# Kernel optimization log

Hardware: AMD Instinct MI355X
Metric: run time of the kernel (lower is better)

Reference implementation:

```python
import jax, jax.numpy as jnp
import numpy as np

B, T, C, H = 32, 512, 8, 256  # batch, seq_len, n_channels, HIDDEN_SIZE
G = 4 * H  # gate dim (i, f, g, o)


def setup_inputs() -> dict:
    key = jax.random.key(0)
    ks = jax.random.split(key, 12)
    k_scale = 1.0 / np.sqrt(H)  # PyTorch LSTM/Linear uniform init bound
    u = lambda k, shape: jax.random.uniform(k, shape, jnp.float32, -k_scale, k_scale)
    return {
        "x": jax.random.normal(ks[0], (B, T, C), jnp.float32),
        # per-channel LSTM layer 1 (input_size=1)
        "Wih1": u(ks[1], (C, G, 1)),
        "Whh1": u(ks[2], (C, G, H)),
        "bih1": u(ks[3], (C, G)),
        "bhh1": u(ks[4], (C, G)),
        # per-channel LSTM layer 2 (input_size=H)
        "Wih2": u(ks[5], (C, G, H)),
        "Whh2": u(ks[6], (C, G, H)),
        "bih2": u(ks[7], (C, G)),
        "bhh2": u(ks[8], (C, G)),
        # per-channel Linear(H, 1)
        "Wlin": u(ks[9], (C, H)),
        "blin": u(ks[10], (C,)),
    }


def _lstm_layer(x_proj, Whh):
    """x_proj: [T, C, B, 4H] precomputed input projection + biases.
    Whh: [C, 4H, H]. Returns hidden states [T, C, B, H]."""
    c_dim, b_dim = x_proj.shape[1], x_proj.shape[2]
    h0 = jnp.zeros((c_dim, b_dim, H), x_proj.dtype)
    c0 = jnp.zeros((c_dim, b_dim, H), x_proj.dtype)

    def step(carry, xp_t):
        h, c = carry
        gates = xp_t + jnp.einsum('cbh,cgh->cbg', h, Whh)
        i, f, g, o = jnp.split(gates, 4, axis=-1)  # PyTorch gate order i,f,g,o
        i = jax.nn.sigmoid(i)
        f = jax.nn.sigmoid(f)
        g = jnp.tanh(g)
        o = jax.nn.sigmoid(o)
        c_new = f * c + i * g
        h_new = o * jnp.tanh(c_new)
        return (h_new, c_new), h_new

    _, hs = jax.lax.scan(step, (h0, c0), x_proj)
    return hs  # [T, C, B, H]


def reference(x, Wih1, Whh1, bih1, bhh1, Wih2, Whh2, bih2, bhh2, Wlin, blin):
    # Dropout layers are identity in eval mode.
    # Layer 1: input_size=1 -> input projection is a per-channel scale of x.
    b1 = (bih1 + bhh1)[None, :, None, :]  # [1, C, 1, 4H]
    xp1 = jnp.einsum('btc,cg->tcbg', x, Wih1[:, :, 0]) + b1  # [T, C, B, 4H]
    h1 = _lstm_layer(xp1, Whh1)  # [T, C, B, H]

    # Layer 2
    b2 = (bih2 + bhh2)[None, :, None, :]
    xp2 = jnp.einsum('tcbh,cgh->tcbg', h1, Wih2) + b2
    h2 = _lstm_layer(xp2, Whh2)  # [T, C, B, H]

    # Per-channel Linear(H, 1), concatenated over channel dim.
    out = jnp.einsum('tcbh,ch->btc', h2, Wlin) + blin[None, None, :]
    return out  # [B, T, C]
```

## Files before the change

### kernel.cpp

```cpp
#include <hip/hip_runtime.h>

#define Bn 32
#define Tn 512
#define Cn 8
#define Hn 256
#define Gn 1024
#define NTHR 256
#define SLC  16
#define NBLK (Cn*2*SLC)
#define K2n  (Hn/2)
#define BUFS 4
#define EXU  (BUFS*Cn*K2n*Bn)
#define GP2  18

typedef __attribute__((ext_vector_type(8))) __bf16 bf16x8;
typedef __attribute__((ext_vector_type(8))) short  short8;
typedef __attribute__((ext_vector_type(4))) float  f32x4;
typedef __attribute__((ext_vector_type(4))) unsigned uintx4;
typedef unsigned long long u64;

__device__ __forceinline__ unsigned bfr(float f) {
    unsigned u = __float_as_uint(f);
    return (u + 0x7fffu + ((u >> 16) & 1u)) >> 16;
}
__device__ __forceinline__ float sigmf(float v)  { return 1.0f / (1.0f + __expf(-v)); }
__device__ __forceinline__ float tanh_f(float v) { return 1.0f - 2.0f / (__expf(2.0f * v) + 1.0f); }

__device__ __forceinline__ f32x4 mf(short8 a, short8 b, f32x4 c) {
    return __builtin_amdgcn_mfma_f32_16x16x32_bf16(
        __builtin_bit_cast(bf16x8, a), __builtin_bit_cast(bf16x8, b), c, 0, 0, 0);
}

__device__ __forceinline__ void splitw(const float* __restrict__ p, short8& hi, short8& lo) {
    short8 h, l;
#pragma unroll
    for (int j = 0; j < 8; ++j) {
        const float v = p[j];
        const unsigned hb = bfr(v);
        h[j] = (short)hb;
        l[j] = (short)bfr(v - __uint_as_float(hb << 16));
    }
    hi = h; lo = l;
}

__device__ __forceinline__ void ast64(u64* p, u64 v) {
    __hip_atomic_store(p, v, __ATOMIC_RELAXED, __HIP_MEMORY_SCOPE_AGENT);
}
__device__ __forceinline__ u64 ald64(const u64* p) {
    return __hip_atomic_load(p, __ATOMIC_RELAXED, __HIP_MEMORY_SCOPE_AGENT);
}

__global__ void __launch_bounds__(NTHR, 1)
lstm_mfma(const float* __restrict__ x,
          const float* __restrict__ Wih1, const float* __restrict__ Whh1,
          const float* __restrict__ bih1, const float* __restrict__ bhh1,
          const float* __restrict__ Wih2, const float* __restrict__ Whh2,
          const float* __restrict__ bih2, const float* __restrict__ bhh2,
          const float* __restrict__ Wlin, const float* __restrict__ blin,
          float* __restrict__ out, void* __restrict__ wsv, int use_part) {
    __shared__ float g1buf[2 * 64 * GP2];
    __shared__ float g2buf[2 * 64 * GP2];
    __shared__ short8 w2lds[4][2][4][2][64];

    u64* EX1 = (u64*)wsv;
    u64* EX2 = EX1 + EXU;
    float* part = (float*)(EX2 + EXU);

    const int tid  = threadIdx.x;
    const int wg   = blockIdx.x;
    const int c    = wg & 7;
    const int s    = (wg >> 3) & 15;
    const int bh   = (wg >> 7) & 1;
    const int lane = tid & 63;
    const int wid  = tid >> 6;
    const int kg   = wid & 1;
    const int mh   = wid >> 1;
    const int n    = lane & 15;
    const int quad = lane >> 4;
    const int bn   = bh * 16 + n;

    short8 w1h[2][4], w1l[2][4], w3h[2][4], w3l[2][4];
#pragma unroll
    for (int mt = 0; mt < 2; ++mt) {
        const int r = mh * 32 + mt * 16 + n;
        const size_t g = (size_t)((r >> 4) * Hn + s * 16 + (r & 15));
        const size_t base = (size_t)c * Gn * Hn + g * Hn + kg * 128 + quad * 8;
#pragma unroll
        for (int kk = 0; kk < 4; ++kk) {
            splitw(Whh1 + base + kk * 32, w1h[mt][kk], w1l[mt][kk]);
            splitw(Whh2 + base + kk * 32, w3h[mt][kk], w3l[mt][kk]);
            short8 t2h, t2l;
            splitw(Wih2 + base + kk * 32, t2h, t2l);
            w2lds[wid][mt][kk][0][lane] = t2h;
            w2lds[wid][mt][kk][1][lane] = t2l;
        }
    }

    float wi1_r[2][4], bs1_r[2][4], bs2_r[2][4];
#pragma unroll
    for (int mt = 0; mt < 2; ++mt)
#pragma unroll
        for (int reg = 0; reg < 4; ++reg) {
            const int r = mh * 32 + mt * 16 + quad * 4 + reg;
            const int g = (r >> 4) * Hn + s * 16 + (r & 15);
            wi1_r[mt][reg] = Wih1[c * Gn + g];
            bs1_r[mt][reg] = bih1[c * Gn + g] + bhh1[c * Gn + g];
            bs2_r[mt][reg] = bih2[c * Gn + g] + bhh2[c * Gn + g];
        }

    const int jj = tid & 15;
    const int bb = tid >> 4;
    const int gb = bh * 16 + bb;
    const float wl = Wlin[c * Hn + s * 16 + jj];
    const float bl = blin[c];

    __syncthreads();

    float c1 = 0.0f, c2 = 0.0f;

    for (int t = 0; t <= Tn; ++t) {
        const bool doA = (t < Tn);
        const bool doB = (t >= 1);

        const float xv = doA ? x[(bn * Tn + t) * Cn + c] : 0.0f;

        const u64* E1 = EX1 + (size_t)(((t + 3) & 3) * Cn + c) * K2n * Bn;
        short8 f1h[4], f1l[4];
        {
            const unsigned ptag = (unsigned)((t + 2) % 3) + 1u;
            const unsigned em = (ptag & 1u) | ((ptag & 2u) << 15);
            const bool chk = (t >= 1);
            for (;;) {
                unsigned bad = 0;
#pragma unroll
                for (int kk = 0; kk < 4; ++kk) {
                    uintx4 ah, al;
#pragma unroll
                    for (int j2 = 0; j2 < 4; ++j2) {
                        const int k2 = kg * 64 + kk * 16 + quad * 4 + j2;
                        const u64 v1 = ald64(E1 + k2 * Bn + bn);
                        ah[j2] = (unsigned)v1;
                        al[j2] = (unsigned)(v1 >> 32);
                        bad |= (al[j2] ^ em) & 0x00010001u;
                    }
                    f1h[kk] = __builtin_bit_cast(short8, ah);
                    f1l[kk] = __builtin_bit_cast(short8, al);
                }
                if (!chk || __all((int)(bad == 0))) break;
                __builtin_amdgcn_s_sleep(1);
            }
        }

        if (doA) {
            f32x4 a1a[2] = {{0,0,0,0},{0,0,0,0}}, a1x[2] = {{0,0,0,0},{0,0,0,0}};
#pragma unroll
            for (int kk = 0; kk < 4; ++kk)
#pragma unroll
                for (int mt = 0; mt < 2; ++mt) {
                    a1a[mt] = mf(w1h[mt][kk], f1h[kk], a1a[mt]);
                    a1x[mt] = mf(w1l[mt][kk], f1h[kk], mf(w1h[mt][kk], f1l[kk], a1x[mt]));
                }
#pragma unroll
            for (int mt = 0; mt < 2; ++mt)
#pragma unroll
                for (int reg = 0; reg < 4; ++reg) {
                    const int r = mh * 32 + mt * 16 + quad * 4 + reg;
                    float e1 = a1a[mt][reg] + a1x[mt][reg];
                    if (kg == 0) e1 += xv * wi1_r[mt][reg] + bs1_r[mt][reg];
                    g1buf[(kg * 64 + r) * GP2 + n] = e1;
                }
        }
        __syncthreads();

        if (doA) {
            const float iv = sigmf (g1buf[jj * GP2 + bb]        + g1buf[(64 + jj) * GP2 + bb]);
            const float fv = sigmf (g1buf[(16 + jj) * GP2 + bb] + g1buf[(80 + jj) * GP2 + bb]);
            const float gv = tanh_f(g1buf[(32 + jj) * GP2 + bb] + g1buf[(96 + jj) * GP2 + bb]);
            const float ov = sigmf (g1buf[(48 + jj) * GP2 + bb] + g1buf[(112 + jj) * GP2 + bb]);
            c1 = fv * c1 + iv * gv;
            const float h1v = ov * tanh_f(c1);
            const unsigned hb = bfr(h1v);
            const unsigned lb = bfr(h1v - __uint_as_float(hb << 16));
            const unsigned packed = (hb << 16) | lb;
            const unsigned nbp = (unsigned)__shfl_xor((int)packed, 1, 64);
            const unsigned ctag = (unsigned)(t % 3) + 1u;
            const unsigned cm = (ctag & 1u) | ((ctag & 2u) << 15);
            if ((jj & 1) == 0) {
                const unsigned hip = (packed >> 16) | (nbp & 0xffff0000u);
                unsigned lop = (packed & 0xffffu) | (nbp << 16);
                lop = (lop & 0xFFFEFFFEu) | cm;
                const int k2 = s * 8 + (jj >> 1);
                ast64(EX1 + (size_t)((t & 3) * Cn + c) * K2n * Bn + k2 * Bn + gb,
                      (u64)hip | ((u64)lop << 32));
            }
        }

        const u64* E2 = EX2 + (size_t)(((t + 2) & 3) * Cn + c) * K2n * Bn;
        u64 r2[4][4];
        if (doB) {
#pragma unroll
            for (int kk = 0; kk < 4; ++kk)
#pragma unroll
                for (int j2 = 0; j2 < 4; ++j2) {
                    const int k2 = kg * 64 + kk * 16 + quad * 4 + j2;
                    r2[kk][j2] = ald64(E2 + k2 * Bn + bn);
                }
        }

        f32x4 a2a[2] = {{0,0,0,0},{0,0,0,0}}, a2x[2] = {{0,0,0,0},{0,0,0,0}};
        if (doB) {
#pragma unroll
            for (int kk = 0; kk < 4; ++kk)
#pragma unroll
                for (int mt = 0; mt < 2; ++mt) {
                    const short8 wh = w2lds[wid][mt][kk][0][lane];
                    const short8 wlo = w2lds[wid][mt][kk][1][lane];
                    a2a[mt] = mf(wh, f1h[kk], a2a[mt]);
                    a2x[mt] = mf(wlo, f1h[kk], mf(wh, f1l[kk], a2x[mt]));
                }
        }

        short8 f2h[4], f2l[4];
        if (doB) {
            const unsigned ptag = (unsigned)((t + 1) % 3) + 1u;
            const unsigned em = (ptag & 1u) | ((ptag & 2u) << 15);
            const bool chk = (t >= 2);
            for (;;) {
                unsigned bad = 0;
#pragma unroll
                for (int kk = 0; kk < 4; ++kk) {
                    uintx4 ah, al;
#pragma unroll
                    for (int j2 = 0; j2 < 4; ++j2) {
                        ah[j2] = (unsigned)r2[kk][j2];
                        al[j2] = (unsigned)(r2[kk][j2] >> 32);
                        bad |= (al[j2] ^ em) & 0x00010001u;
                    }
                    f2h[kk] = __builtin_bit_cast(short8, ah);
                    f2l[kk] = __builtin_bit_cast(short8, al);
                }
                if (!chk || __all((int)(bad == 0))) break;
                __builtin_amdgcn_s_sleep(1);
#pragma unroll
                for (int kk = 0; kk < 4; ++kk)
#pragma unroll
                    for (int j2 = 0; j2 < 4; ++j2) {
                        const int k2 = kg * 64 + kk * 16 + quad * 4 + j2;
                        r2[kk][j2] = ald64(E2 + k2 * Bn + bn);
                    }
            }
        }

        if (doB) {
#pragma unroll
            for (int kk = 0; kk < 4; ++kk)
#pragma unroll
                for (int mt = 0; mt < 2; ++mt) {
                    a2a[mt] = mf(w3h[mt][kk], f2h[kk], a2a[mt]);
                    a2x[mt] = mf(w3l[mt][kk], f2h[kk], mf(w3h[mt][kk], f2l[kk], a2x[mt]));
                }
#pragma unroll
            for (int mt = 0; mt < 2; ++mt)
#pragma unroll
                for (int reg = 0; reg < 4; ++reg) {
                    const int r = mh * 32 + mt * 16 + quad * 4 + reg;
                    float e2 = a2a[mt][reg] + a2x[mt][reg];
                    if (kg == 0) e2 += bs2_r[mt][reg];
                    g2buf[(kg * 64 + r) * GP2 + n] = e2;
                }
        }
        __syncthreads();

        if (doB) {
            const float iv = sigmf (g2buf[jj * GP2 + bb]        + g2buf[(64 + jj) * GP2 + bb]);
            const float fv = sigmf (g2buf[(16 + jj) * GP2 + bb] + g2buf[(80 + jj) * GP2 + bb]);
            const float gv = tanh_f(g2buf[(32 + jj) * GP2 + bb] + g2buf[(96 + jj) * GP2 + bb]);
            const float ov = sigmf (g2buf[(48 + jj) * GP2 + bb] + g2buf[(112 + jj) * GP2 + bb]);
            c2 = fv * c2 + iv * gv;
            const float h2v = ov * tanh_f(c2);
            const unsigned hb = bfr(h2v);
            const unsigned lb = bfr(h2v - __uint_as_float(hb << 16));
            const unsigned packed = (hb << 16) | lb;
            const unsigned nbp = (unsigned)__shfl_xor((int)packed, 1, 64);
            const unsigned ctag = (unsigned)((t + 2) % 3) + 1u;
            const unsigned cm = (ctag & 1u) | ((ctag & 2u) << 15);
            if (t < Tn && (jj & 1) == 0) {
                const unsigned hip = (packed >> 16) | (nbp & 0xffff0000u);
                unsigned lop = (packed & 0xffffu) | (nbp << 16);
                lop = (lop & 0xFFFEFFFEu) | cm;
                const int k2 = s * 8 + (jj >> 1);
                ast64(EX2 + (size_t)(((t + 3) & 3) * Cn + c) * K2n * Bn + k2 * Bn + gb,
                      (u64)hip | ((u64)lop << 32));
            }

            float pv = h2v * wl;
            pv += __shfl_xor(pv, 1, 64);
            pv += __shfl_xor(pv, 2, 64);
            pv += __shfl_xor(pv, 4, 64);
            pv += __shfl_xor(pv, 8, 64);
            if (jj == 0) {
                if (use_part) {
                    part[(((t - 1) * Cn + c) * SLC + s) * Bn + gb] = pv;
                } else {
                    atomicAdd(&out[(gb * Tn + (t - 1)) * Cn + c], pv + (s == 0 ? bl : 0.0f));
                }
            }
        }
    }
}

__global__ void reduce_out(const float* __restrict__ part, const float* __restrict__ blin,
                           float* __restrict__ out) {
    const int t = blockIdx.x;
    const int c = threadIdx.x >> 5;
    const int b = threadIdx.x & 31;
    float v = blin[c];
#pragma unroll
    for (int s = 0; s < SLC; ++s) v += part[((t * Cn + c) * SLC + s) * Bn + b];
    out[(b * Tn + t) * Cn + c] = v;
}

extern "C" void kernel_launch(void* const* d_in, const int* in_sizes, int n_in,
                              void* d_out, int out_size, void* d_ws, size_t ws_size,
                              hipStream_t stream) {
    const float* x    = (const float*)d_in[0];
    const float* Wih1 = (const float*)d_in[1];
    const float* Whh1 = (const float*)d_in[2];
    const float* bih1 = (const float*)d_in[3];
    const float* bhh1 = (const float*)d_in[4];
    const float* Wih2 = (const float*)d_in[5];
    const float* Whh2 = (const float*)d_in[6];
    const float* bih2 = (const float*)d_in[7];
    const float* bhh2 = (const float*)d_in[8];
    const float* Wlin = (const float*)d_in[9];
    const float* blin = (const float*)d_in[10];
    float* out = (float*)d_out;

    const size_t h_bytes    = (size_t)2 * EXU * sizeof(u64);
    const size_t part_bytes = (size_t)Tn * Cn * SLC * Bn * sizeof(float);
    const int use_part = (ws_size >= h_bytes + part_bytes) ? 1 : 0;

    hipMemsetAsync(d_ws, 0, h_bytes, stream);
    if (!use_part)
        hipMemsetAsync(d_out, 0, (size_t)out_size * sizeof(float), stream);

    lstm_mfma<<<NBLK, NTHR, 0, stream>>>(
        x, Wih1, Whh1, bih1, bhh1, Wih2, Whh2, bih2, bhh2, Wlin, blin, out, d_ws, use_part);

    if (use_part) {
        const float* part = (const float*)((const char*)d_ws + h_bytes);
        reduce_out<<<Tn, Cn * Bn, 0, stream>>>(part, blin, out);
    }
}
```

Before: 1.960 ms.

## Split layer-1 and layer-2 LSTM into decoupled warp roles with LDS flag handoff

Doubles the block to 512 threads and gives layer 1 (plus the layer-2 input projection) to four waves and the layer-2 recurrence to another four. The two roles hand off the projection through a tagged LDS ring buffer with progress counters instead of block-wide barriers. Each wave now owns whole gate columns, so activations come from a small per-wave LDS transpose rather than a cross-wave reduction. The intent is to take layer 2 off layer 1's critical path and drop per-step __syncthreads. The cost is more registers per thread, spin-wait polling, and four times as many partial sums for the final reduction.

```diff
diff --git a/kernel.cpp b/kernel.cpp
--- a/kernel.cpp
+++ b/kernel.cpp
@@ -5,13 +5,13 @@
 #define Cn 8
 #define Hn 256
 #define Gn 1024
-#define NTHR 256
+#define NTHR 512
 #define SLC  16
 #define NBLK (Cn*2*SLC)
 #define K2n  (Hn/2)
 #define BUFS 4
 #define EXU  (BUFS*Cn*K2n*Bn)
-#define GP2  18
+#define SLC4 (SLC*4)
 
 typedef __attribute__((ext_vector_type(8))) __bf16 bf16x8;
 typedef __attribute__((ext_vector_type(8))) short  short8;
@@ -49,8 +49,14 @@
 __device__ __forceinline__ u64 ald64(const u64* p) {
     return __hip_atomic_load(p, __ATOMIC_RELAXED, __HIP_MEMORY_SCOPE_AGENT);
 }
-
-__global__ void __launch_bounds__(NTHR, 1)
+__device__ __forceinline__ void astw(unsigned* p, unsigned v) {
+    __hip_atomic_store(p, v, __ATOMIC_RELAXED, __HIP_MEMORY_SCOPE_WORKGROUP);
+}
+__device__ __forceinline__ unsigned aldw(const unsigned* p) {
+    return __hip_atomic_load(p, __ATOMIC_RELAXED, __HIP_MEMORY_SCOPE_WORKGROUP);
+}
+
+__global__ void __launch_bounds__(NTHR, 2)
 lstm_mfma(const float* __restrict__ x,
           const float* __restrict__ Wih1, const float* __restrict__ Whh1,
           const float* __restrict__ bih1, const float* __restrict__ bhh1,
@@ -58,9 +64,10 @@
           const float* __restrict__ bih2, const float* __restrict__ bhh2,
           const float* __restrict__ Wlin, const float* __restrict__ blin,
           float* __restrict__ out, void* __restrict__ wsv, int use_part) {
-    __shared__ float g1buf[2 * 64 * GP2];
-    __shared__ float g2buf[2 * 64 * GP2];
-    __shared__ short8 w2lds[4][2][4][2][64];
+    __shared__ short8  w2lds[4][8][2][64];
+    __shared__ float   tbuf[8][16][20];
+    __shared__ unsigned xp2b[4][4][16][16];
+    __shared__ unsigned prog[4];
 
     u64* EX1 = (u64*)wsv;
     u64* EX2 = EX1 + EXU;
@@ -73,74 +80,60 @@
     const int bh   = (wg >> 7) & 1;
     const int lane = tid & 63;
     const int wid  = tid >> 6;
-    const int kg   = wid & 1;
-    const int mh   = wid >> 1;
+    const int role = wid >> 2;
+    const int w    = wid & 3;
     const int n    = lane & 15;
-    const int quad = lane >> 4;
+    const int q    = lane >> 4;
     const int bn   = bh * 16 + n;
 
-    short8 w1h[2][4], w1l[2][4], w3h[2][4], w3l[2][4];
-#pragma unroll
-    for (int mt = 0; mt < 2; ++mt) {
-        const int r = mh * 32 + mt * 16 + n;
-        const size_t g = (size_t)((r >> 4) * Hn + s * 16 + (r & 15));
-        const size_t base = (size_t)c * Gn * Hn + g * Hn + kg * 128 + quad * 8;
-#pragma unroll
-        for (int kk = 0; kk < 4; ++kk) {
-            splitw(Whh1 + base + kk * 32, w1h[mt][kk], w1l[mt][kk]);
-            splitw(Whh2 + base + kk * 32, w3h[mt][kk], w3l[mt][kk]);
-            short8 t2h, t2l;
-            splitw(Wih2 + base + kk * 32, t2h, t2l);
-            w2lds[wid][mt][kk][0][lane] = t2h;
-            w2lds[wid][mt][kk][1][lane] = t2l;
-        }
-    }
-
-    float wi1_r[2][4], bs1_r[2][4], bs2_r[2][4];
-#pragma unroll
-    for (int mt = 0; mt < 2; ++mt)
-#pragma unroll
-        for (int reg = 0; reg < 4; ++reg) {
-            const int r = mh * 32 + mt * 16 + quad * 4 + reg;
-            const int g = (r >> 4) * Hn + s * 16 + (r & 15);
-            wi1_r[mt][reg] = Wih1[c * Gn + g];
-            bs1_r[mt][reg] = bih1[c * Gn + g] + bhh1[c * Gn + g];
-            bs2_r[mt][reg] = bih2[c * Gn + g] + bhh2[c * Gn + g];
-        }
-
-    const int jj = tid & 15;
-    const int bb = tid >> 4;
-    const int gb = bh * 16 + bb;
-    const float wl = Wlin[c * Hn + s * 16 + jj];
-    const float bl = blin[c];
-
-    __syncthreads();
-
-    float c1 = 0.0f, c2 = 0.0f;
-
-    for (int t = 0; t <= Tn; ++t) {
-        const bool doA = (t < Tn);
-        const bool doB = (t >= 1);
-
-        const float xv = doA ? x[(bn * Tn + t) * Cn + c] : 0.0f;
-
-        const u64* E1 = EX1 + (size_t)(((t + 3) & 3) * Cn + c) * K2n * Bn;
-        short8 f1h[4], f1l[4];
-        {
+    for (int i = tid; i < 4 * 4 * 16 * 16; i += NTHR) ((unsigned*)xp2b)[i] = 0u;
+    if (tid < 4) prog[tid] = 0u;
+
+    const int grow = ((n >> 2) << 8) + s * 16 + w * 4 + (n & 3);
+    const size_t wbase = (size_t)c * Gn * Hn + (size_t)grow * Hn + q * 8;
+
+    if (role == 0) {
+        short8 w1h[8], w1l[8];
+#pragma unroll
+        for (int kk = 0; kk < 8; ++kk) {
+            splitw(Whh1 + wbase + kk * 32, w1h[kk], w1l[kk]);
+            short8 th, tl;
+            splitw(Wih2 + wbase + kk * 32, th, tl);
+            w2lds[w][kk][0][lane] = th;
+            w2lds[w][kk][1][lane] = tl;
+        }
+        float wi1c[4], bs1c[4];
+#pragma unroll
+        for (int tt = 0; tt < 4; ++tt) {
+            const int g = tt * 256 + s * 16 + w * 4 + q;
+            wi1c[tt] = Wih1[c * Gn + g];
+            bs1c[tt] = bih1[c * Gn + g] + bhh1[c * Gn + g];
+        }
+        float* tb = &tbuf[wid][0][0];
+        __syncthreads();
+
+        float c1 = 0.0f;
+        for (int t = 0; t <= Tn; ++t) {
+            const bool doCell = (t < Tn);
+            unsigned pg = aldw(&prog[w]);
+            const float xv = doCell ? x[((size_t)bn * Tn + t) * Cn + c] : 0.0f;
+
+            const u64* E1r = EX1 + (size_t)(((t + 3) & 3) * Cn + c) * K2n * Bn;
             const unsigned ptag = (unsigned)((t + 2) % 3) + 1u;
             const unsigned em = (ptag & 1u) | ((ptag & 2u) << 15);
             const bool chk = (t >= 1);
+            short8 f1h[8], f1l[8];
             for (;;) {
                 unsigned bad = 0;
 #pragma unroll
-                for (int kk = 0; kk < 4; ++kk) {
+                for (int kk = 0; kk < 8; ++kk) {
                     uintx4 ah, al;
 #pragma unroll
                     for (int j2 = 0; j2 < 4; ++j2) {
-                        const int k2 = kg * 64 + kk * 16 + quad * 4 + j2;
-                        const u64 v1 = ald64(E1 + k2 * Bn + bn);
-                        ah[j2] = (unsigned)v1;
-                        al[j2] = (unsigned)(v1 >> 32);
+                        const int k2 = kk * 16 + q * 4 + j2;
+                        const u64 v = ald64(E1r + k2 * Bn + bn);
+                        ah[j2] = (unsigned)v;
+                        al[j2] = (unsigned)(v >> 32);
                         bad |= (al[j2] ^ em) & 0x00010001u;
                     }
                     f1h[kk] = __builtin_bit_cast(short8, ah);
@@ -149,91 +142,100 @@
                 if (!chk || __all((int)(bad == 0))) break;
                 __builtin_amdgcn_s_sleep(1);
             }
-        }
-
-        if (doA) {
-            f32x4 a1a[2] = {{0,0,0,0},{0,0,0,0}}, a1x[2] = {{0,0,0,0},{0,0,0,0}};
-#pragma unroll
-            for (int kk = 0; kk < 4; ++kk)
-#pragma unroll
-                for (int mt = 0; mt < 2; ++mt) {
-                    a1a[mt] = mf(w1h[mt][kk], f1h[kk], a1a[mt]);
-                    a1x[mt] = mf(w1l[mt][kk], f1h[kk], mf(w1h[mt][kk], f1l[kk], a1x[mt]));
-                }
-#pragma unroll
-            for (int mt = 0; mt < 2; ++mt)
-#pragma unroll
-                for (int reg = 0; reg < 4; ++reg) {
-                    const int r = mh * 32 + mt * 16 + quad * 4 + reg;
-                    float e1 = a1a[mt][reg] + a1x[mt][reg];
-                    if (kg == 0) e1 += xv * wi1_r[mt][reg] + bs1_r[mt][reg];
-                    g1buf[(kg * 64 + r) * GP2 + n] = e1;
-                }
-        }
+
+            if (doCell) {
+                f32x4 aa = {0,0,0,0}, ax = {0,0,0,0};
+#pragma unroll
+                for (int kk = 0; kk < 8; ++kk) {
+                    aa = mf(w1h[kk], f1h[kk], aa);
+                    ax = mf(w1l[kk], f1h[kk], mf(w1h[kk], f1l[kk], ax));
+                }
+#pragma unroll
+                for (int r = 0; r < 4; ++r) tb[n * 20 + q * 4 + r] = aa[r] + ax[r];
+                asm volatile("s_waitcnt lgkmcnt(0)" ::: "memory");
+                float gv[4];
+#pragma unroll
+                for (int tt = 0; tt < 4; ++tt) gv[tt] = tb[n * 20 + tt * 4 + q];
+
+                const float iv = sigmf (gv[0] + xv * wi1c[0] + bs1c[0]);
+                const float fv = sigmf (gv[1] + xv * wi1c[1] + bs1c[1]);
+                const float gg = tanh_f(gv[2] + xv * wi1c[2] + bs1c[2]);
+                const float ov = sigmf (gv[3] + xv * wi1c[3] + bs1c[3]);
+                c1 = fv * c1 + iv * gg;
+                const float h1v = ov * tanh_f(c1);
+
+                const unsigned hb = bfr(h1v);
+                const unsigned lb = bfr(h1v - __uint_as_float(hb << 16));
+                const unsigned packed = (hb << 16) | lb;
+                const unsigned nbp = (unsigned)__shfl_xor((int)packed, 16, 64);
+                const unsigned ctag = (unsigned)(t % 3) + 1u;
+                const unsigned cm = (ctag & 1u) | ((ctag & 2u) << 15);
+                if ((q & 1) == 0) {
+                    const unsigned hip = (packed >> 16) | (nbp & 0xffff0000u);
+                    unsigned lop = (packed & 0xffffu) | (nbp << 16);
+                    lop = (lop & 0xFFFEFFFEu) | cm;
+                    const int k2p = s * 8 + w * 2 + (q >> 1);
+                    ast64(EX1 + (size_t)((t & 3) * Cn + c) * K2n * Bn + k2p * Bn + bn,
+                          (u64)hip | ((u64)lop << 32));
+                }
+            }
+
+            if (t >= 1) {
+                f32x4 aa2 = {0,0,0,0}, ax2 = {0,0,0,0};
+#pragma unroll
+                for (int kk = 0; kk < 8; ++kk) {
+                    const short8 wh = w2lds[w][kk][0][lane];
+                    const short8 wl8 = w2lds[w][kk][1][lane];
+                    aa2 = mf(wh, f1h[kk], aa2);
+                    ax2 = mf(wl8, f1h[kk], mf(wh, f1l[kk], ax2));
+                }
+                while ((int)pg < t - 4) {
+                    __builtin_amdgcn_s_sleep(2);
+                    pg = aldw(&prog[w]);
+                }
+                const unsigned utag = (unsigned)((t - 1) % 3) + 1u;
+                unsigned* dst = &xp2b[w][(t - 1) & 3][n][q * 4];
+#pragma unroll
+                for (int r = 0; r < 4; ++r) {
+                    const unsigned b = __float_as_uint(aa2[r] + ax2[r]);
+                    astw(dst + r, (b & ~3u) | utag);
+                }
+            }
+        }
+    } else {
+        short8 w3h[8], w3l[8];
+#pragma unroll
+        for (int kk = 0; kk < 8; ++kk)
+            splitw(Whh2 + wbase + kk * 32, w3h[kk], w3l[kk]);
+        float bs2c[4];
+#pragma unroll
+        for (int tt = 0; tt < 4; ++tt) {
+            const int g = tt * 256 + s * 16 + w * 4 + q;
+            bs2c[tt] = bih2[c * Gn + g] + bhh2[c * Gn + g];
+        }
+        const float wl = Wlin[c * Hn + s * 16 + w * 4 + q];
+        const float bl = blin[c];
+        float* tb = &tbuf[wid][0][0];
         __syncthreads();
 
-        if (doA) {
-            const float iv = sigmf (g1buf[jj * GP2 + bb]        + g1buf[(64 + jj) * GP2 + bb]);
-            const float fv = sigmf (g1buf[(16 + jj) * GP2 + bb] + g1buf[(80 + jj) * GP2 + bb]);
-            const float gv = tanh_f(g1buf[(32 + jj) * GP2 + bb] + g1buf[(96 + jj) * GP2 + bb]);
-            const float ov = sigmf (g1buf[(48 + jj) * GP2 + bb] + g1buf[(112 + jj) * GP2 + bb]);
-            c1 = fv * c1 + iv * gv;
-            const float h1v = ov * tanh_f(c1);
-            const unsigned hb = bfr(h1v);
-            const unsigned lb = bfr(h1v - __uint_as_float(hb << 16));
-            const unsigned packed = (hb << 16) | lb;
-            const unsigned nbp = (unsigned)__shfl_xor((int)packed, 1, 64);
-            const unsigned ctag = (unsigned)(t % 3) + 1u;
-            const unsigned cm = (ctag & 1u) | ((ctag & 2u) << 15);
-            if ((jj & 1) == 0) {
-                const unsigned hip = (packed >> 16) | (nbp & 0xffff0000u);
-                unsigned lop = (packed & 0xffffu) | (nbp << 16);
-                lop = (lop & 0xFFFEFFFEu) | cm;
-                const int k2 = s * 8 + (jj >> 1);
-                ast64(EX1 + (size_t)((t & 3) * Cn + c) * K2n * Bn + k2 * Bn + gb,
-                      (u64)hip | ((u64)lop << 32));
-            }
-        }
-
-        const u64* E2 = EX2 + (size_t)(((t + 2) & 3) * Cn + c) * K2n * Bn;
-        u64 r2[4][4];
-        if (doB) {
-#pragma unroll
-            for (int kk = 0; kk < 4; ++kk)
-#pragma unroll
-                for (int j2 = 0; j2 < 4; ++j2) {
-                    const int k2 = kg * 64 + kk * 16 + quad * 4 + j2;
-                    r2[kk][j2] = ald64(E2 + k2 * Bn + bn);
-                }
-        }
-
-        f32x4 a2a[2] = {{0,0,0,0},{0,0,0,0}}, a2x[2] = {{0,0,0,0},{0,0,0,0}};
-        if (doB) {
-#pragma unroll
-            for (int kk = 0; kk < 4; ++kk)
-#pragma unroll
-                for (int mt = 0; mt < 2; ++mt) {
-                    const short8 wh = w2lds[wid][mt][kk][0][lane];
-                    const short8 wlo = w2lds[wid][mt][kk][1][lane];
-                    a2a[mt] = mf(wh, f1h[kk], a2a[mt]);
-                    a2x[mt] = mf(wlo, f1h[kk], mf(wh, f1l[kk], a2x[mt]));
-                }
-        }
-
-        short8 f2h[4], f2l[4];
-        if (doB) {
-            const unsigned ptag = (unsigned)((t + 1) % 3) + 1u;
+        float c2 = 0.0f;
+        for (int u = 0; u < Tn; ++u) {
+            const u64* E2r = EX2 + (size_t)(((u + 3) & 3) * Cn + c) * K2n * Bn;
+            const unsigned ptag = (unsigned)((u + 2) % 3) + 1u;
             const unsigned em = (ptag & 1u) | ((ptag & 2u) << 15);
-            const bool chk = (t >= 2);
+            const bool chk = (u >= 1);
+            short8 f2h[8], f2l[8];
             for (;;) {
                 unsigned bad = 0;
 #pragma unroll
-                for (int kk = 0; kk < 4; ++kk) {
+                for (int kk = 0; kk < 8; ++kk) {
                     uintx4 ah, al;
 #pragma unroll
                     for (int j2 = 0; j2 < 4; ++j2) {
-                        ah[j2] = (unsigned)r2[kk][j2];
-                        al[j2] = (unsigned)(r2[kk][j2] >> 32);
+                        const int k2 = kk * 16 + q * 4 + j2;
+                        const u64 v = ald64(E2r + k2 * Bn + bn);
+                        ah[j2] = (unsigned)v;
+                        al[j2] = (unsigned)(v >> 32);
                         bad |= (al[j2] ^ em) & 0x00010001u;
                     }
                     f2h[kk] = __builtin_bit_cast(short8, ah);
@@ -241,68 +243,66 @@
                 }
                 if (!chk || __all((int)(bad == 0))) break;
                 __builtin_amdgcn_s_sleep(1);
-#pragma unroll
-                for (int kk = 0; kk < 4; ++kk)
-#pragma unroll
-                    for (int j2 = 0; j2 < 4; ++j2) {
-                        const int k2 = kg * 64 + kk * 16 + quad * 4 + j2;
-                        r2[kk][j2] = ald64(E2 + k2 * Bn + bn);
-                    }
-            }
-        }
-
-        if (doB) {
-#pragma unroll
-            for (int kk = 0; kk < 4; ++kk)
-#pragma unroll
-                for (int mt = 0; mt < 2; ++mt) {
-                    a2a[mt] = mf(w3h[mt][kk], f2h[kk], a2a[mt]);
-                    a2x[mt] = mf(w3l[mt][kk], f2h[kk], mf(w3h[mt][kk], f2l[kk], a2x[mt]));
-                }
-#pragma unroll
-            for (int mt = 0; mt < 2; ++mt)
-#pragma unroll
-                for (int reg = 0; reg < 4; ++reg) {
-                    const int r = mh * 32 + mt * 16 + quad * 4 + reg;
-                    float e2 = a2a[mt][reg] + a2x[mt][reg];
-                    if (kg == 0) e2 += bs2_r[mt][reg];
-                    g2buf[(kg * 64 + r) * GP2 + n] = e2;
-                }
-        }
-        __syncthreads();
-
-        if (doB) {
-            const float iv = sigmf (g2buf[jj * GP2 + bb]        + g2buf[(64 + jj) * GP2 + bb]);
-            const float fv = sigmf (g2buf[(16 + jj) * GP2 + bb] + g2buf[(80 + jj) * GP2 + bb]);
-            const float gv = tanh_f(g2buf[(32 + jj) * GP2 + bb] + g2buf[(96 + jj) * GP2 + bb]);
-            const float ov = sigmf (g2buf[(48 + jj) * GP2 + bb] + g2buf[(112 + jj) * GP2 + bb]);
-            c2 = fv * c2 + iv * gv;
+            }
+
+            f32x4 aa = {0,0,0,0}, ax = {0,0,0,0};
+#pragma unroll
+            for (int kk = 0; kk < 8; ++kk) {
+                aa = mf(w3h[kk], f2h[kk], aa);
+                ax = mf(w3l[kk], f2h[kk], mf(w3h[kk], f2l[kk], ax));
+            }
+#pragma unroll
+            for (int r = 0; r < 4; ++r) tb[n * 20 + q * 4 + r] = aa[r] + ax[r];
+            asm volatile("s_waitcnt lgkmcnt(0)" ::: "memory");
+            float gv[4];
+#pragma unroll
+            for (int tt = 0; tt < 4; ++tt) gv[tt] = tb[n * 20 + tt * 4 + q];
+
+            const unsigned etag = (unsigned)(u % 3) + 1u;
+            const unsigned* src = &xp2b[w][u & 3][n][0];
+            unsigned bw0, bw1, bw2, bw3;
+            for (;;) {
+                bw0 = aldw(src + 0 * 4 + q);
+                bw1 = aldw(src + 1 * 4 + q);
+                bw2 = aldw(src + 2 * 4 + q);
+                bw3 = aldw(src + 3 * 4 + q);
+                const unsigned bad = ((bw0 & 3u) ^ etag) | ((bw1 & 3u) ^ etag) |
+                                     ((bw2 & 3u) ^ etag) | ((bw3 & 3u) ^ etag);
+                if (__all((int)(bad == 0))) break;
+                __builtin_amdgcn_s_sleep(1);
+            }
+            astw(&prog[w], (unsigned)(u + 1));
+
+            const float iv = sigmf (gv[0] + __uint_as_float(bw0) + bs2c[0]);
+            const float fv = sigmf (gv[1] + __uint_as_float(bw1) + bs2c[1]);
+            const float gg = tanh_f(gv[2] + __uint_as_float(bw2) + bs2c[2]);
+            const float ov = sigmf (gv[3] + __uint_as_float(bw3) + bs2c[3]);
+            c2 = fv * c2 + iv * gg;
             const float h2v = ov * tanh_f(c2);
+
             const unsigned hb = bfr(h2v);
             const unsigned lb = bfr(h2v - __uint_as_float(hb << 16));
             const unsigned packed = (hb << 16) | lb;
-            const unsigned nbp = (unsigned)__shfl_xor((int)packed, 1, 64);
-            const unsigned ctag = (unsigned)((t + 2) % 3) + 1u;
-            const unsigned cm = (ctag & 1u) | ((ctag & 2u) << 15);
-            if (t < Tn && (jj & 1) == 0) {
+            const unsigned nbp = (unsigned)__shfl_xor((int)packed, 16, 64);
+            if (u < Tn - 1 && (q & 1) == 0) {
+                const unsigned cm = (etag & 1u) | ((etag & 2u) << 15);
                 const unsigned hip = (packed >> 16) | (nbp & 0xffff0000u);
                 unsigned lop = (packed & 0xffffu) | (nbp << 16);
                 lop = (lop & 0xFFFEFFFEu) | cm;
-                const int k2 = s * 8 + (jj >> 1);
-                ast64(EX2 + (size_t)(((t + 3) & 3) * Cn + c) * K2n * Bn + k2 * Bn + gb,
+                const int k2p = s * 8 + w * 2 + (q >> 1);
+                ast64(EX2 + (size_t)((u & 3) * Cn + c) * K2n * Bn + k2p * Bn + bn,
                       (u64)hip | ((u64)lop << 32));
             }
 
             float pv = h2v * wl;
-            pv += __shfl_xor(pv, 1, 64);
-            pv += __shfl_xor(pv, 2, 64);
-            pv += __shfl_xor(pv, 4, 64);
-            pv += __shfl_xor(pv, 8, 64);
-            if (jj == 0) {
+            pv += __shfl_xor(pv, 16, 64);
+            pv += __shfl_xor(pv, 32, 64);
+            if (q == 0) {
                 if (use_part) {
-                    part[(((t - 1) * Cn + c) * SLC + s) * Bn + gb] = pv;
+                    part[(((size_t)u * Cn + c) * SLC4 + (s * 4 + w)) * Bn + bn] = pv;
                 } else {
-                    atomicAdd(&out[(gb * Tn + (t - 1)) * Cn + c], pv + (s == 0 ? bl : 0.0f));
+                    atomicAdd(&out[((size_t)bn * Tn + u) * Cn + c],
+                              pv + ((s == 0 && w == 0) ? bl : 0.0f));
                 }
             }
         }
@@ -316,7 +316,8 @@
     const int b = threadIdx.x & 31;
     float v = blin[c];
 #pragma unroll
-    for (int s = 0; s < SLC; ++s) v += part[((t * Cn + c) * SLC + s) * Bn + b];
+    for (int s4 = 0; s4 < SLC4; ++s4)
+        v += part[(((size_t)t * Cn + c) * SLC4 + s4) * Bn + b];
     out[(b * Tn + t) * Cn + c] = v;
 }
 
@@ -337,7 +338,7 @@
     float* out = (float*)d_out;
 
     const size_t h_bytes    = (size_t)2 * EXU * sizeof(u64);
-    const size_t part_bytes = (size_t)Tn * Cn * SLC * Bn * sizeof(float);
+    const size_t part_bytes = (size_t)Tn * Cn * SLC4 * Bn * sizeof(float);
     const int use_part = (ws_size >= h_bytes + part_bytes) ? 1 : 0;
 
     hipMemsetAsync(d_ws, 0, h_bytes, stream);
```

Measured after the change: 2.291 ms. 16.9% more time.
